# Optimization experiments

Hardware: AMD Instinct MI355X
Metric: run time of the kernel (lower is better)

The kernel has to match this reference:

```python
import math
import jax, jax.numpy as jnp
import numpy as np

H = 32          # query heads
KV = 8          # key/value heads (GQA)
D = 128         # head_dim
PAGE = 16       # Quest page size
TOPK = 256      # page budget
THETA = 10000.0


def _rope(x, pos):
    # x: [..., D]; llama rotate_half RoPE at scalar position pos
    half = D // 2
    inv = 1.0 / (THETA ** (jnp.arange(half, dtype=jnp.float32) * 2.0 / D))
    ang = pos * inv                                   # [half]
    cos = jnp.concatenate([jnp.cos(ang), jnp.cos(ang)])  # [D]
    sin = jnp.concatenate([jnp.sin(ang), jnp.sin(ang)])
    rot = jnp.concatenate([-x[..., half:], x[..., :half]], axis=-1)
    return x * cos + rot * sin


def setup_inputs() -> dict:
    key = jax.random.key(0)
    ks = jax.random.split(key, 7)
    hid = H * D
    s = 1.0 / math.sqrt(hid)
    return {
        "hidden_states": jax.random.normal(ks[0], (1, 1, hid), jnp.float32),
        "k_cache": jax.random.normal(ks[1], (32767, KV, D), jnp.float32),
        "v_cache": jax.random.normal(ks[2], (32767, KV, D), jnp.float32),
        "Wq": jax.random.normal(ks[3], (hid, H * D), jnp.float32) * s,
        "Wk": jax.random.normal(ks[4], (hid, KV * D), jnp.float32) * s,
        "Wv": jax.random.normal(ks[5], (hid, KV * D), jnp.float32) * s,
        "Wo": jax.random.normal(ks[6], (H * D, hid), jnp.float32) * s,
    }


def reference(hidden_states, k_cache, v_cache, Wq, Wk, Wv, Wo):
    x = hidden_states[0]                    # [1, hidden]
    q = (x @ Wq).reshape(H, D)              # decode: q_len == 1
    k = (x @ Wk).reshape(KV, D)
    v = (x @ Wv).reshape(KV, D)

    past = k_cache.shape[0]
    q = _rope(q, jnp.float32(past))
    k = _rope(k, jnp.float32(past))

    # append_kv: paged cache, seqlen = past + 1 = n_pages * PAGE
    Kc = jnp.concatenate([k_cache, k[None]], axis=0)   # [S, KV, D]
    Vc = jnp.concatenate([v_cache, v[None]], axis=0)
    S = past + 1
    n_pages = S // PAGE

    # decode_estimate: per-page min/max key metadata, Quest upper-bound score
    Kp = Kc.reshape(n_pages, PAGE, KV, D)
    kmax = Kp.max(axis=1)                   # [P, KV, D]
    kmin = Kp.min(axis=1)
    G = H // KV
    qh = q.reshape(KV, G, D)
    pmax = qh[None] * kmax[:, :, None, :]   # [P, KV, G, D]
    pmin = qh[None] * kmin[:, :, None, :]
    score = jnp.maximum(pmax, pmin).sum(-1) # [P, KV, G]
    score = score.reshape(n_pages, H).T     # [H, P]
    # most recent page always attended
    score = score.at[:, -1].set(jnp.inf)

    # decode_topk: per-head page selection
    _, pidx = jax.lax.top_k(score, TOPK)    # [H, TOPK]
    tok = (pidx[..., None] * PAGE + jnp.arange(PAGE)).reshape(H, -1)  # [H, T]

    # decode_sparse_attn: gather selected pages (GQA mapping) + attention
    kvmap = jnp.arange(H) // G              # query head -> kv head
    Ksel = Kc[tok, kvmap[:, None]]          # [H, T, D]
    Vsel = Vc[tok, kvmap[:, None]]
    att = jnp.einsum('hd,htd->ht', q, Ksel) * (1.0 / math.sqrt(D))
    w = jax.nn.softmax(att, axis=-1)
    out = jnp.einsum('ht,htd->hd', w, Vsel) # [H, D]

    y = out.reshape(1, H * D) @ Wo          # o_proj
    return y[None]                          # [1, 1, hidden]
```

## Files before the change

kernel.cpp:

```cpp
#include <hip/hip_runtime.h>
#include <math.h>

#define H 32
#define KV 8
#define D 128
#define PAGE 16
#define TOPK 256
#define NPAGES 2048
#define PAST 32767
#define HID 4096

#define WS_Q       0
#define WS_K       4096
#define WS_V       5120
#define WS_ROPE    6144
#define WS_SCORES  6272
#define WS_PIDX    71808
#define WS_PART_M  80000
#define WS_PART_L  81024
#define WS_PART_O  82048
#define WS_KMAX    213120
#define WS_KMIN    2310272
#define WS_QKVPART 4407424
#define WS_WOPART  5193856

#define NCHUNK 32
#define PPC    8

__global__ void fused1_kernel(const float* __restrict__ x,
                              const float* __restrict__ Wq,
                              const float* __restrict__ Wk,
                              const float* __restrict__ Wv,
                              const float* __restrict__ kc,
                              float* __restrict__ ws) {
    __shared__ float xs[32];
    int tid = threadIdx.x;
    int b = blockIdx.x;
    if (b < 768) {
        int rc = b / 6;
        int cg = b % 6;
        int r0 = rc * 32;
        if (tid < 32) xs[tid] = x[r0 + tid];
        __syncthreads();
        const float* W; int Cc; int col; int gcol;
        if (cg < 4)       { W = Wq; Cc = 4096; col = cg * 1024 + tid * 4; gcol = col; }
        else if (cg == 4) { W = Wk; Cc = 1024; col = tid * 4;             gcol = 4096 + col; }
        else              { W = Wv; Cc = 1024; col = tid * 4;             gcol = 5120 + col; }
        const float* Wp = W + (size_t)r0 * Cc + col;
        float4 acc = {0.f, 0.f, 0.f, 0.f};
#pragma unroll 8
        for (int r = 0; r < 32; ++r) {
            float4 w4 = *(const float4*)(Wp + (size_t)r * Cc);
            float xr = xs[r];
            acc.x = fmaf(xr, w4.x, acc.x);
            acc.y = fmaf(xr, w4.y, acc.y);
            acc.z = fmaf(xr, w4.z, acc.z);
            acc.w = fmaf(xr, w4.w, acc.w);
        }
        *(float4*)(ws + WS_QKVPART + (size_t)rc * 6144 + gcol) = acc;
    } else if (b < 768 + (NPAGES - 1)) {
        int p = b - 768;
        int kv = tid >> 5;
        int sub = tid & 31;
        const float* kp = kc + ((size_t)(p * PAGE) * KV + kv) * D + 4 * sub;
        float4 mx = {-INFINITY, -INFINITY, -INFINITY, -INFINITY};
        float4 mn = { INFINITY,  INFINITY,  INFINITY,  INFINITY};
#pragma unroll
        for (int t = 0; t < PAGE; ++t) {
            float4 v = *(const float4*)(kp + (size_t)t * (KV * D));
            mx.x = fmaxf(mx.x, v.x); mn.x = fminf(mn.x, v.x);
            mx.y = fmaxf(mx.y, v.y); mn.y = fminf(mn.y, v.y);
            mx.z = fmaxf(mx.z, v.z); mn.z = fminf(mn.z, v.z);
            mx.w = fmaxf(mx.w, v.w); mn.w = fminf(mn.w, v.w);
        }
        size_t o = ((size_t)p * KV + kv) * D + 4 * sub;
        *(float4*)(ws + WS_KMAX + o) = mx;
        *(float4*)(ws + WS_KMIN + o) = mn;
    } else {
        if (tid < 64) {
            double t = (double)tid / 64.0;
            float pw = (float)pow(10000.0, t);
            float invf = 1.0f / pw;
            float ang = 32767.0f * invf;
            ws[WS_ROPE + tid]      = (float)cos((double)ang);
            ws[WS_ROPE + 64 + tid] = (float)sin((double)ang);
        }
    }
}

__global__ void reduce_rope_kernel(const float* __restrict__ part,
                                   const float* __restrict__ rope,
                                   float* __restrict__ qkv) {
    __shared__ float smem[256];
    int tid = threadIdx.x;
    int c = blockIdx.x * 256 + tid;
    float s = 0.f;
#pragma unroll 8
    for (int rc = 0; rc < 128; ++rc) s += part[(size_t)rc * 6144 + c];
    smem[tid] = s;
    __syncthreads();
    float outv;
    if (c < 5120) {
        int j = c & 127;
        int jj = j & 63;
        float co = rope[jj];
        float si = rope[64 + jj];
        if (j < 64) { float x0 = s, x1 = smem[tid + 64]; outv = x0 * co - x1 * si; }
        else        { float x1 = s, x0 = smem[tid - 64]; outv = x1 * co + x0 * si; }
    } else {
        outv = s;
    }
    qkv[c] = outv;
}

__global__ void score_kernel(const float* __restrict__ kmaxb,
                             const float* __restrict__ kminb,
                             const float* __restrict__ q,
                             float* __restrict__ scores) {
    int tid = threadIdx.x;
    int pl = tid & 7;
    int h  = tid >> 3;
    int kv = h >> 2;
    int p  = blockIdx.x * 8 + pl;
    if (p >= NPAGES - 1) return;
    const float* qp  = q + (size_t)h * D;
    const float* kmx = kmaxb + ((size_t)p * KV + kv) * D;
    const float* kmn = kminb + ((size_t)p * KV + kv) * D;
    float acc = 0.f;
#pragma unroll 8
    for (int d0 = 0; d0 < 32; ++d0) {
        float4 qq = *(const float4*)(qp + 4 * d0);
        float4 a  = *(const float4*)(kmx + 4 * d0);
        float4 bb = *(const float4*)(kmn + 4 * d0);
        acc += fmaxf(qq.x * a.x, qq.x * bb.x) + fmaxf(qq.y * a.y, qq.y * bb.y)
             + fmaxf(qq.z * a.z, qq.z * bb.z) + fmaxf(qq.w * a.w, qq.w * bb.w);
    }
    scores[(size_t)h * NPAGES + p] = acc;
}

__global__ void topk_kernel(const float* __restrict__ scores, int* __restrict__ pidx) {
    __shared__ unsigned su[NPAGES];
    __shared__ int hist[256];
    __shared__ int scan[256];
    __shared__ int wtot[4];
    __shared__ int cnt;
    __shared__ unsigned s_prefix;
    __shared__ int s_k;
    int tid = threadIdx.x;
    int lane = tid & 63;
    int wv = tid >> 6;
    int h = blockIdx.x;
    for (int i = tid; i < NPAGES; i += 256) {
        unsigned u;
        if (i == NPAGES - 1) u = 0xFFFFFFFFu;
        else {
            int b = __float_as_int(scores[(size_t)h * NPAGES + i]);
            u = (b >= 0) ? ((unsigned)b | 0x80000000u) : ~(unsigned)b;
        }
        su[i] = u;
    }
    if (tid == 0) cnt = 0;
    __syncthreads();

    unsigned prefix = 0;
    int K = TOPK;
    for (int level = 3; level >= 0; --level) {
        int shift = level * 8;
        unsigned pmask = (level == 3) ? 0u : (0xFFFFFFFFu << (shift + 8));
        hist[tid] = 0;
        __syncthreads();
        for (int i = tid; i < NPAGES; i += 256) {
            unsigned u = su[i];
            if ((u & pmask) == prefix)
                atomicAdd(&hist[(u >> shift) & 0xFF], 1);
        }
        __syncthreads();
        int v = hist[tid];
#pragma unroll
        for (int off = 1; off < 64; off <<= 1) {
            int o = __shfl_down(v, off);
            if (lane + off < 64) v += o;
        }
        if (lane == 0) wtot[wv] = v;
        __syncthreads();
        int add = 0;
        for (int w2 = wv + 1; w2 < 4; ++w2) add += wtot[w2];
        v += add;
        scan[tid] = v;
        __syncthreads();
        int nxt = (tid < 255) ? scan[tid + 1] : 0;
        if (v >= K && nxt < K) {
            s_prefix = prefix | ((unsigned)tid << shift);
            s_k = K - nxt;
        }
        __syncthreads();
        prefix = s_prefix;
        K = s_k;
        __syncthreads();
    }
    unsigned T = prefix;

    for (int i = tid; i < NPAGES; i += 256) {
        if (su[i] > T) {
            int pos = atomicAdd(&cnt, 1);
            pidx[h * TOPK + pos] = i;
        }
    }
    int base = TOPK - K;
    int i0 = tid * (NPAGES / 256);
    int tcount = 0;
#pragma unroll
    for (int j = 0; j < NPAGES / 256; ++j) if (su[i0 + j] == T) ++tcount;
    int sc = tcount;
#pragma unroll
    for (int off = 1; off < 64; off <<= 1) {
        int o = __shfl_up(sc, off);
        if (lane >= off) sc += o;
    }
    __syncthreads();
    if (lane == 63) wtot[wv] = sc;
    __syncthreads();
    int wadd = 0;
    for (int w2 = 0; w2 < wv; ++w2) wadd += wtot[w2];
    int pos = base + (sc - tcount) + wadd;
#pragma unroll
    for (int j = 0; j < NPAGES / 256; ++j) {
        if (su[i0 + j] == T) {
            if (pos < TOPK) pidx[h * TOPK + pos] = i0 + j;
            ++pos;
        }
    }
}

__global__ void attn_kernel(const float* __restrict__ kc,
                            const float* __restrict__ vc,
                            const float* __restrict__ ws,
                            const int* __restrict__ pidx,
                            float* __restrict__ part_m,
                            float* __restrict__ part_l,
                            float* __restrict__ part_o) {
    int tid = threadIdx.x;
    int lane = tid & 63;
    int wv = tid >> 6;
    int sub = lane & 31;
    int hf = lane >> 5;
    int h = blockIdx.x >> 5;
    int c = blockIdx.x & 31;
    int kvh = h >> 2;
    __shared__ float qs[128];
    __shared__ float sm[8], sl[8];
    __shared__ float so[8 * 128];
    if (tid < 128) qs[tid] = ws[WS_Q + h * 128 + tid];
    __syncthreads();
    float4 q4 = *(const float4*)(qs + 4 * sub);
    int hidx = wv * 2 + hf;
    int page = pidx[h * TOPK + c * PPC + hidx];
    size_t base = ((size_t)(page * PAGE) * KV + kvh) * D + 4 * sub;
    bool last = (page == NPAGES - 1);
    const float scale = 0.08838834764831843f;

    float s[PAGE];
#pragma unroll
    for (int t = 0; t < PAGE; ++t) {
        const float* kp = (last && t == PAGE - 1) ? (ws + WS_K + kvh * 128 + 4 * sub)
                                                  : (kc + base + (size_t)t * (KV * D));
        float4 kk = *(const float4*)kp;
        float d = q4.x * kk.x + q4.y * kk.y + q4.z * kk.z + q4.w * kk.w;
#pragma unroll
        for (int off = 16; off > 0; off >>= 1) d += __shfl_xor(d, off);
        s[t] = d * scale;
    }
    float m = -INFINITY;
#pragma unroll
    for (int t = 0; t < PAGE; ++t) m = fmaxf(m, s[t]);
    float l = 0.f;
    float4 o = {0.f, 0.f, 0.f, 0.f};
#pragma unroll
    for (int t = 0; t < PAGE; ++t) {
        float w = __expf(s[t] - m);
        l += w;
        const float* vp = (last && t == PAGE - 1) ? (ws + WS_V + kvh * 128 + 4 * sub)
                                                  : (vc + base + (size_t)t * (KV * D));
        float4 vv = *(const float4*)vp;
        o.x = fmaf(w, vv.x, o.x);
        o.y = fmaf(w, vv.y, o.y);
        o.z = fmaf(w, vv.z, o.z);
        o.w = fmaf(w, vv.w, o.w);
    }
    if (sub == 0) { sm[hidx] = m; sl[hidx] = l; }
    *(float4*)(so + hidx * 128 + 4 * sub) = o;
    __syncthreads();
    if (tid < 128) {
        float M = -INFINITY;
#pragma unroll
        for (int w2 = 0; w2 < 8; ++w2) M = fmaxf(M, sm[w2]);
        float L = 0.f, O = 0.f;
#pragma unroll
        for (int w2 = 0; w2 < 8; ++w2) {
            float f = __expf(sm[w2] - M);
            L += f * sl[w2];
            O += f * so[w2 * 128 + tid];
        }
        int pc = h * NCHUNK + c;
        if (tid == 0) { part_m[pc] = M; part_l[pc] = L; }
        part_o[(size_t)pc * 128 + tid] = O;
    }
}

__global__ void wo1_kernel(const float* __restrict__ part_m,
                           const float* __restrict__ part_l,
                           const float* __restrict__ part_o,
                           const float* __restrict__ Wo,
                           float* __restrict__ wpart) {
    __shared__ float xs[32];
    int tid = threadIdx.x;
    int rc = blockIdx.x >> 2;
    int cb = blockIdx.x & 3;
    int r0 = rc * 32;
    int h0 = r0 >> 7;
    int dbase = r0 & 127;
    if (tid < 32) {
        int d = dbase + tid;
        float M = -INFINITY;
#pragma unroll
        for (int c = 0; c < NCHUNK; ++c) M = fmaxf(M, part_m[h0 * NCHUNK + c]);
        float L = 0.f, O = 0.f;
#pragma unroll
        for (int c = 0; c < NCHUNK; ++c) {
            float f = __expf(part_m[h0 * NCHUNK + c] - M);
            L += f * part_l[h0 * NCHUNK + c];
            O += f * part_o[(size_t)(h0 * NCHUNK + c) * 128 + d];
        }
        xs[tid] = O / L;
    }
    __syncthreads();
    int col = cb * 1024 + tid * 4;
    const float* Wp = Wo + (size_t)r0 * 4096 + col;
    float4 acc = {0.f, 0.f, 0.f, 0.f};
#pragma unroll 8
    for (int r = 0; r < 32; ++r) {
        float4 w4 = *(const float4*)(Wp + (size_t)r * 4096);
        float xr = xs[r];
        acc.x = fmaf(xr, w4.x, acc.x);
        acc.y = fmaf(xr, w4.y, acc.y);
        acc.z = fmaf(xr, w4.z, acc.z);
        acc.w = fmaf(xr, w4.w, acc.w);
    }
    *(float4*)(wpart + (size_t)rc * 4096 + col) = acc;
}

__global__ void wo2_kernel(const float* __restrict__ wpart,
                           float* __restrict__ out) {
    int tid = threadIdx.x;
    int col = blockIdx.x * 256 + tid;
    float acc = 0.f;
#pragma unroll 8
    for (int rc = 0; rc < 128; ++rc) acc += wpart[(size_t)rc * 4096 + col];
    out[col] = acc;
}

extern "C" void kernel_launch(void* const* d_in, const int* in_sizes, int n_in,
                              void* d_out, int out_size, void* d_ws, size_t ws_size,
                              hipStream_t stream) {
    const float* x  = (const float*)d_in[0];
    const float* kc = (const float*)d_in[1];
    const float* vc = (const float*)d_in[2];
    const float* Wq = (const float*)d_in[3];
    const float* Wk = (const float*)d_in[4];
    const float* Wv = (const float*)d_in[5];
    const float* Wo = (const float*)d_in[6];
    float* ws = (float*)d_ws;
    float* out = (float*)d_out;

    fused1_kernel<<<768 + (NPAGES - 1) + 1, 256, 0, stream>>>(x, Wq, Wk, Wv, kc, ws);
    reduce_rope_kernel<<<24, 256, 0, stream>>>(ws + WS_QKVPART, ws + WS_ROPE, ws + WS_Q);
    score_kernel<<<256, 256, 0, stream>>>(ws + WS_KMAX, ws + WS_KMIN, ws + WS_Q, ws + WS_SCORES);
    topk_kernel<<<H, 256, 0, stream>>>(ws + WS_SCORES, (int*)(ws + WS_PIDX));
    attn_kernel<<<H * NCHUNK, 256, 0, stream>>>(kc, vc, ws, (const int*)(ws + WS_PIDX),
                                                ws + WS_PART_M, ws + WS_PART_L, ws + WS_PART_O);
    wo1_kernel<<<512, 256, 0, stream>>>(ws + WS_PART_M, ws + WS_PART_L, ws + WS_PART_O,
                                        Wo, ws + WS_WOPART);
    wo2_kernel<<<16, 256, 0, stream>>>(ws + WS_WOPART, out);
}
```

Measured before the change: 417.5 us.

## Batch global loads for memory-level parallelism and restructure score kernel per page

Several kernels (QKV projection, K page min/max, partial-sum reductions, attention, Wo projection) now issue all of their independent global loads into register arrays before computing, so more memory requests are in flight per thread. The score kernel is remapped to one block per page: each thread loads its kmax/kmin slice once and reuses it across the four query heads of its GQA group, reducing with wavefront shuffles. The old mapping re-read the per-page metadata with strided per-thread loads. The larger register arrays may raise register pressure and lower occupancy.

```diff
diff --git a/kernel.cpp b/kernel.cpp
--- a/kernel.cpp
+++ b/kernel.cpp
@@ -48,14 +48,20 @@
         else              { W = Wv; Cc = 1024; col = tid * 4;             gcol = 5120 + col; }
         const float* Wp = W + (size_t)r0 * Cc + col;
         float4 acc = {0.f, 0.f, 0.f, 0.f};
-#pragma unroll 8
-        for (int r = 0; r < 32; ++r) {
-            float4 w4 = *(const float4*)(Wp + (size_t)r * Cc);
-            float xr = xs[r];
-            acc.x = fmaf(xr, w4.x, acc.x);
-            acc.y = fmaf(xr, w4.y, acc.y);
-            acc.z = fmaf(xr, w4.z, acc.z);
-            acc.w = fmaf(xr, w4.w, acc.w);
+#pragma unroll
+        for (int rb = 0; rb < 32; rb += 16) {
+            float4 w4[16];
+#pragma unroll
+            for (int j = 0; j < 16; ++j)
+                w4[j] = *(const float4*)(Wp + (size_t)(rb + j) * Cc);
+#pragma unroll
+            for (int j = 0; j < 16; ++j) {
+                float xr = xs[rb + j];
+                acc.x = fmaf(xr, w4[j].x, acc.x);
+                acc.y = fmaf(xr, w4[j].y, acc.y);
+                acc.z = fmaf(xr, w4[j].z, acc.z);
+                acc.w = fmaf(xr, w4[j].w, acc.w);
+            }
         }
         *(float4*)(ws + WS_QKVPART + (size_t)rc * 6144 + gcol) = acc;
     } else if (b < 768 + (NPAGES - 1)) {
@@ -63,15 +69,18 @@
         int kv = tid >> 5;
         int sub = tid & 31;
         const float* kp = kc + ((size_t)(p * PAGE) * KV + kv) * D + 4 * sub;
-        float4 mx = {-INFINITY, -INFINITY, -INFINITY, -INFINITY};
-        float4 mn = { INFINITY,  INFINITY,  INFINITY,  INFINITY};
-#pragma unroll
-        for (int t = 0; t < PAGE; ++t) {
-            float4 v = *(const float4*)(kp + (size_t)t * (KV * D));
-            mx.x = fmaxf(mx.x, v.x); mn.x = fminf(mn.x, v.x);
-            mx.y = fmaxf(mx.y, v.y); mn.y = fminf(mn.y, v.y);
-            mx.z = fmaxf(mx.z, v.z); mn.z = fminf(mn.z, v.z);
-            mx.w = fmaxf(mx.w, v.w); mn.w = fminf(mn.w, v.w);
+        float4 vbuf[16];
+#pragma unroll
+        for (int t = 0; t < PAGE; ++t)
+            vbuf[t] = *(const float4*)(kp + (size_t)t * (KV * D));
+        float4 mx = vbuf[0];
+        float4 mn = vbuf[0];
+#pragma unroll
+        for (int t = 1; t < PAGE; ++t) {
+            mx.x = fmaxf(mx.x, vbuf[t].x); mn.x = fminf(mn.x, vbuf[t].x);
+            mx.y = fmaxf(mx.y, vbuf[t].y); mn.y = fminf(mn.y, vbuf[t].y);
+            mx.z = fmaxf(mx.z, vbuf[t].z); mn.z = fminf(mn.z, vbuf[t].z);
+            mx.w = fmaxf(mx.w, vbuf[t].w); mn.w = fminf(mn.w, vbuf[t].w);
         }
         size_t o = ((size_t)p * KV + kv) * D + 4 * sub;
         *(float4*)(ws + WS_KMAX + o) = mx;
@@ -95,8 +104,13 @@
     int tid = threadIdx.x;
     int c = blockIdx.x * 256 + tid;
     float s = 0.f;
-#pragma unroll 8
-    for (int rc = 0; rc < 128; ++rc) s += part[(size_t)rc * 6144 + c];
+    for (int rb = 0; rb < 128; rb += 16) {
+        float v[16];
+#pragma unroll
+        for (int j = 0; j < 16; ++j) v[j] = part[(size_t)(rb + j) * 6144 + c];
+#pragma unroll
+        for (int j = 0; j < 16; ++j) s += v[j];
+    }
     smem[tid] = s;
     __syncthreads();
     float outv;
@@ -118,24 +132,26 @@
                              const float* __restrict__ q,
                              float* __restrict__ scores) {
     int tid = threadIdx.x;
-    int pl = tid & 7;
-    int h  = tid >> 3;
-    int kv = h >> 2;
-    int p  = blockIdx.x * 8 + pl;
-    if (p >= NPAGES - 1) return;
-    const float* qp  = q + (size_t)h * D;
-    const float* kmx = kmaxb + ((size_t)p * KV + kv) * D;
-    const float* kmn = kminb + ((size_t)p * KV + kv) * D;
-    float acc = 0.f;
-#pragma unroll 8
-    for (int d0 = 0; d0 < 32; ++d0) {
-        float4 qq = *(const float4*)(qp + 4 * d0);
-        float4 a  = *(const float4*)(kmx + 4 * d0);
-        float4 bb = *(const float4*)(kmn + 4 * d0);
-        acc += fmaxf(qq.x * a.x, qq.x * bb.x) + fmaxf(qq.y * a.y, qq.y * bb.y)
-             + fmaxf(qq.z * a.z, qq.z * bb.z) + fmaxf(qq.w * a.w, qq.w * bb.w);
-    }
-    scores[(size_t)h * NPAGES + p] = acc;
+    int kv = tid >> 5;
+    int sub = tid & 31;
+    int p = blockIdx.x;
+    size_t o = ((size_t)p * KV + kv) * D + 4 * sub;
+    float4 mx = *(const float4*)(kmaxb + o);
+    float4 mn = *(const float4*)(kminb + o);
+    float4 qq[4];
+#pragma unroll
+    for (int g = 0; g < 4; ++g)
+        qq[g] = *(const float4*)(q + (size_t)(kv * 4 + g) * D + 4 * sub);
+#pragma unroll
+    for (int g = 0; g < 4; ++g) {
+        float sacc = fmaxf(qq[g].x * mx.x, qq[g].x * mn.x)
+                   + fmaxf(qq[g].y * mx.y, qq[g].y * mn.y)
+                   + fmaxf(qq[g].z * mx.z, qq[g].z * mn.z)
+                   + fmaxf(qq[g].w * mx.w, qq[g].w * mn.w);
+#pragma unroll
+        for (int off = 16; off > 0; off >>= 1) sacc += __shfl_xor(sacc, off);
+        if (sub == 0) scores[(size_t)(kv * 4 + g) * NPAGES + p] = sacc;
+    }
 }
 
 __global__ void topk_kernel(const float* __restrict__ scores, int* __restrict__ pidx) {
@@ -259,13 +275,17 @@
     bool last = (page == NPAGES - 1);
     const float scale = 0.08838834764831843f;
 
-    float s[PAGE];
+    float4 kk[PAGE];
 #pragma unroll
     for (int t = 0; t < PAGE; ++t) {
         const float* kp = (last && t == PAGE - 1) ? (ws + WS_K + kvh * 128 + 4 * sub)
                                                   : (kc + base + (size_t)t * (KV * D));
-        float4 kk = *(const float4*)kp;
-        float d = q4.x * kk.x + q4.y * kk.y + q4.z * kk.z + q4.w * kk.w;
+        kk[t] = *(const float4*)kp;
+    }
+    float s[PAGE];
+#pragma unroll
+    for (int t = 0; t < PAGE; ++t) {
+        float d = q4.x * kk[t].x + q4.y * kk[t].y + q4.z * kk[t].z + q4.w * kk[t].w;
 #pragma unroll
         for (int off = 16; off > 0; off >>= 1) d += __shfl_xor(d, off);
         s[t] = d * scale;
@@ -273,19 +293,24 @@
     float m = -INFINITY;
 #pragma unroll
     for (int t = 0; t < PAGE; ++t) m = fmaxf(m, s[t]);
+
+    float4 vv[PAGE];
+#pragma unroll
+    for (int t = 0; t < PAGE; ++t) {
+        const float* vp = (last && t == PAGE - 1) ? (ws + WS_V + kvh * 128 + 4 * sub)
+                                                  : (vc + base + (size_t)t * (KV * D));
+        vv[t] = *(const float4*)vp;
+    }
     float l = 0.f;
     float4 o = {0.f, 0.f, 0.f, 0.f};
 #pragma unroll
     for (int t = 0; t < PAGE; ++t) {
         float w = __expf(s[t] - m);
         l += w;
-        const float* vp = (last && t == PAGE - 1) ? (ws + WS_V + kvh * 128 + 4 * sub)
-                                                  : (vc + base + (size_t)t * (KV * D));
-        float4 vv = *(const float4*)vp;
-        o.x = fmaf(w, vv.x, o.x);
-        o.y = fmaf(w, vv.y, o.y);
-        o.z = fmaf(w, vv.z, o.z);
-        o.w = fmaf(w, vv.w, o.w);
+        o.x = fmaf(w, vv[t].x, o.x);
+        o.y = fmaf(w, vv[t].y, o.y);
+        o.z = fmaf(w, vv[t].z, o.z);
+        o.w = fmaf(w, vv[t].w, o.w);
     }
     if (sub == 0) { sm[hidx] = m; sl[hidx] = l; }
     *(float4*)(so + hidx * 128 + 4 * sub) = o;
@@ -337,14 +362,20 @@
     int col = cb * 1024 + tid * 4;
     const float* Wp = Wo + (size_t)r0 * 4096 + col;
     float4 acc = {0.f, 0.f, 0.f, 0.f};
-#pragma unroll 8
-    for (int r = 0; r < 32; ++r) {
-        float4 w4 = *(const float4*)(Wp + (size_t)r * 4096);
-        float xr = xs[r];
-        acc.x = fmaf(xr, w4.x, acc.x);
-        acc.y = fmaf(xr, w4.y, acc.y);
-        acc.z = fmaf(xr, w4.z, acc.z);
-        acc.w = fmaf(xr, w4.w, acc.w);
+#pragma unroll
+    for (int rb = 0; rb < 32; rb += 16) {
+        float4 w4[16];
+#pragma unroll
+        for (int j = 0; j < 16; ++j)
+            w4[j] = *(const float4*)(Wp + (size_t)(rb + j) * 4096);
+#pragma unroll
+        for (int j = 0; j < 16; ++j) {
+            float xr = xs[rb + j];
+            acc.x = fmaf(xr, w4[j].x, acc.x);
+            acc.y = fmaf(xr, w4[j].y, acc.y);
+            acc.z = fmaf(xr, w4[j].z, acc.z);
+            acc.w = fmaf(xr, w4[j].w, acc.w);
+        }
     }
     *(float4*)(wpart + (size_t)rc * 4096 + col) = acc;
 }
@@ -354,8 +385,13 @@
     int tid = threadIdx.x;
     int col = blockIdx.x * 256 + tid;
     float acc = 0.f;
-#pragma unroll 8
-    for (int rc = 0; rc < 128; ++rc) acc += wpart[(size_t)rc * 4096 + col];
+    for (int rb = 0; rb < 128; rb += 16) {
+        float v[16];
+#pragma unroll
+        for (int j = 0; j < 16; ++j) v[j] = wpart[(size_t)(rb + j) * 4096 + col];
+#pragma unroll
+        for (int j = 0; j < 16; ++j) acc += v[j];
+    }
     out[col] = acc;
 }
 
@@ -374,7 +410,7 @@
 
     fused1_kernel<<<768 + (NPAGES - 1) + 1, 256, 0, stream>>>(x, Wq, Wk, Wv, kc, ws);
     reduce_rope_kernel<<<24, 256, 0, stream>>>(ws + WS_QKVPART, ws + WS_ROPE, ws + WS_Q);
-    score_kernel<<<256, 256, 0, stream>>>(ws + WS_KMAX, ws + WS_KMIN, ws + WS_Q, ws + WS_SCORES);
+    score_kernel<<<NPAGES - 1, 256, 0, stream>>>(ws + WS_KMAX, ws + WS_KMIN, ws + WS_Q, ws + WS_SCORES);
     topk_kernel<<<H, 256, 0, stream>>>(ws + WS_SCORES, (int*)(ws + WS_PIDX));
     attn_kernel<<<H * NCHUNK, 256, 0, stream>>>(kc, vc, ws, (const int*)(ws + WS_PIDX),
                                                 ws + WS_PART_M, ws + WS_PART_L, ws + WS_PART_O);
```

Result: no change. 415.3 us (-0.5%).
